# Kernel tuning notes

Hardware: AMD Instinct MI355X
Metric: run time of the kernel (lower is better)

## Reference

```python
import jax, jax.numpy as jnp
import numpy as np

B, D, L, H = 256, 256, 256, 512  # batch, driving series (input_size), (T-1)*features_num, hidden_size


def setup_inputs() -> dict:
    key = jax.random.key(0)
    ks = jax.random.split(key, 6)
    s = 1.0 / np.sqrt(H).astype(np.float32)
    return {
        "input_data": jax.random.normal(ks[0], (B, D, L), jnp.float32),
        # attn_linear: Linear(2H + L -> 1)
        "W_attn": jax.random.normal(ks[1], (2 * H + L, 1), jnp.float32) * 0.02,
        "b_attn": jnp.zeros((1,), jnp.float32),
        # single-layer LSTM params, torch gate order (i, f, g, o)
        "W_ih": jax.random.uniform(ks[2], (4 * H, D), jnp.float32, -s, s),
        "W_hh": jax.random.uniform(ks[3], (4 * H, H), jnp.float32, -s, s),
        "b_ih": jax.random.uniform(ks[4], (4 * H,), jnp.float32, -s, s),
        "b_hh": jnp.zeros((4 * H,), jnp.float32),
    }


def reference(input_data, W_attn, b_attn, W_ih, W_hh, b_ih, b_hh):
    Bn, Dn, Ln = input_data.shape
    Hn = W_hh.shape[1]
    # Split attn weight instead of materializing concat([h, c, x]) each step:
    # score = [h | c | x_hist] @ W_attn + b == h@Wh + c@Wc + x_hist@Wx + b
    Wh = W_attn[:Hn, 0]
    Wc = W_attn[Hn:2 * Hn, 0]
    Wx = W_attn[2 * Hn:, 0]
    # x-history contribution is constant across steps -> hoist out of the scan
    x_proj = jnp.einsum("bdl,l->bd", input_data, Wx) + b_attn[0]  # [B, D]
    bias = b_ih + b_hh
    xs = jnp.moveaxis(input_data, 2, 0)  # [L, B, D] per-step columns x_t

    def step(carry, xt):
        h, c = carry  # [B, H] each
        score = x_proj + (h @ Wh + c @ Wc)[:, None]  # [B, D]
        attn = jax.nn.softmax(score, axis=1)  # softmax over driving series
        w = attn * xt  # attention-weighted input, [B, D]
        gates = w @ W_ih.T + h @ W_hh.T + bias  # [B, 4H]
        i, f, g, o = jnp.split(gates, 4, axis=1)
        c2 = jax.nn.sigmoid(f) * c + jax.nn.sigmoid(i) * jnp.tanh(g)
        h2 = jax.nn.sigmoid(o) * jnp.tanh(c2)
        return (h2, c2), (w, h2)

    h0 = jnp.zeros((Bn, Hn), input_data.dtype)
    c0 = jnp.zeros((Bn, Hn), input_data.dtype)
    _, (ws, hs) = jax.lax.scan(step, (h0, c0), xs)
    # match torch's final permute: [total_x_features, B, *] -> [B, total_x_features, *]
    return jnp.moveaxis(ws, 0, 1), jnp.moveaxis(hs, 0, 1)
```

## Files before the change

### kernel.cpp

```cpp
#include <hip/hip_runtime.h>
#include <hip/hip_fp16.h>

typedef _Float16 half8 __attribute__((ext_vector_type(8)));
typedef float floatx4 __attribute__((ext_vector_type(4)));
typedef int intx4 __attribute__((ext_vector_type(4)));

#define NB 256
#define ND 256
#define NL 256
#define NH 512

__global__ void k_xproj(const float* __restrict__ x, const float* __restrict__ Wattn,
                        float* __restrict__ xproj) {
    __shared__ float wx[NL];
    const int tid = threadIdx.x;
    wx[tid] = Wattn[2 * NH + tid];
    __syncthreads();
    const int wid = tid >> 6, lane = tid & 63;
    const int row = blockIdx.x * 4 + wid;
    const float4 v = ((const float4*)(x + (size_t)row * NL))[lane];
    float s = v.x * wx[lane * 4] + v.y * wx[lane * 4 + 1] +
              v.z * wx[lane * 4 + 2] + v.w * wx[lane * 4 + 3];
    #pragma unroll
    for (int off = 32; off; off >>= 1) s += __shfl_down(s, off);
    if (lane == 0) xproj[row] = s;
}

__global__ void k_softmax(const float* __restrict__ xproj, float* __restrict__ attn) {
    const int b = blockIdx.x, tid = threadIdx.x;
    __shared__ float red[8];
    float v = xproj[b * ND + tid];
    float m = v;
    #pragma unroll
    for (int off = 32; off; off >>= 1) m = fmaxf(m, __shfl_down(m, off));
    const int wid = tid >> 6, lane = tid & 63;
    if (lane == 0) red[wid] = m;
    __syncthreads();
    if (tid == 0) {
        float mm = fmaxf(fmaxf(red[0], red[1]), fmaxf(red[2], red[3]));
        red[4] = mm;
    }
    __syncthreads();
    const float e = expf(v - red[4]);
    float s = e;
    #pragma unroll
    for (int off = 32; off; off >>= 1) s += __shfl_down(s, off);
    if (lane == 0) red[wid] = s;
    __syncthreads();
    if (tid == 0) red[5] = red[0] + red[1] + red[2] + red[3];
    __syncthreads();
    attn[b * ND + tid] = e / red[5];
}

__global__ void k_trans(const float* __restrict__ x, const float* __restrict__ attn,
                        float* __restrict__ ws_out, _Float16* __restrict__ w16) {
    __shared__ float tile[64][65];
    const int bid = blockIdx.x;
    const int b = bid >> 4, ti = (bid >> 2) & 3, tj = bid & 3;
    const int tx = threadIdx.x & 63, ty = threadIdx.x >> 6;
    const int d0 = ti * 64, l0 = tj * 64;
    const float* xb = x + ((size_t)b * ND + d0) * NL + l0;
    #pragma unroll
    for (int r = ty; r < 64; r += 4) tile[r][tx] = xb[(size_t)r * NL + tx];
    __syncthreads();
    const float af = attn[b * ND + d0 + tx];
    #pragma unroll
    for (int r = ty; r < 64; r += 4) {
        const int tt = l0 + r;
        const float val = af * tile[tx][r];
        ws_out[((size_t)b * NL + tt) * ND + d0 + tx] = val;
        w16[((size_t)tt * NB + b) * ND + d0 + tx] = (_Float16)val;
    }
}

__global__ void k_wsplit(const float* __restrict__ Whh, const float* __restrict__ Wih,
                         _Float16* __restrict__ hi, _Float16* __restrict__ lo,
                         _Float16* __restrict__ wih16) {
    const int idx = blockIdx.x * 256 + threadIdx.x;
    const float w = Whh[idx];
    const _Float16 h = (_Float16)w;
    hi[idx] = h;
    lo[idx] = (_Float16)(w - (float)h);
    if (idx < 4 * NH * ND) wih16[idx] = (_Float16)Wih[idx];
}

__launch_bounds__(512, 2)
__global__ void k_recur(const _Float16* __restrict__ whhHi, const _Float16* __restrict__ whhLo,
                        const _Float16* __restrict__ wih16, const _Float16* __restrict__ w16,
                        const float* __restrict__ b_ih, const float* __restrict__ b_hh,
                        unsigned int* __restrict__ h32,
                        float* __restrict__ out_hs)
{
    __shared__ char smem[40960];
    const int tid = threadIdx.x;
    const int wid = tid >> 6, lane = tid & 63;
    const int bid = blockIdx.x;
    const int m = bid & 15, hb = bid >> 4;
    const int b0 = m * 16;
    const int gate = wid >> 1, half = wid & 1;
    const int jb = gate * 512 + hb * 32 + half * 16;

    half8 bhhH[16], bhhL[16], bihF[8];
    const int bcol = jb + (lane & 15);
    const int krow = (lane >> 4) * 8;
    #pragma unroll
    for (int kk = 0; kk < 16; ++kk) {
        bhhH[kk] = *(const half8*)(whhHi + (size_t)bcol * NH + kk * 32 + krow);
        bhhL[kk] = *(const half8*)(whhLo + (size_t)bcol * NH + kk * 32 + krow);
    }
    #pragma unroll
    for (int kk = 0; kk < 8; ++kk)
        bihF[kk] = *(const half8*)(wih16 + (size_t)bcol * ND + kk * 32 + krow);

    const int bl = tid >> 5, hl = tid & 31;
    float bias_[4];
    #pragma unroll
    for (int g = 0; g < 4; ++g) {
        const int j = g * 512 + hb * 32 + hl;
        bias_[g] = b_ih[j] + b_hh[j];
    }
    float c = 0.f;
    float* hsOut = out_hs + (size_t)(b0 + bl) * NL * NH + hb * 32 + hl;
    unsigned int* hWr = h32 + (size_t)(b0 + bl) * NH + hb * 32 + hl;

    const int arow = lane & 15;
    const int aq = (lane >> 4) * 16;
    const int aswz = (arow & 7) << 4;

    const int hrow = tid >> 5;
    const int hcol16 = (tid & 31) * 16;
    const int hbase = (hrow << 10) + (tid & 31) * 32;
    const int hswz = (hrow & 7) << 4;

    {
        const char* wsrc = (const char*)(w16 + (size_t)b0 * ND);
        const intx4 wd = *(const intx4*)(wsrc + tid * 16);
        const int wr = tid >> 5;
        *(intx4*)(smem + 16384 + ((tid * 16) ^ ((wr & 7) << 4))) = wd;
    }
    __syncthreads();

    #pragma unroll 1
    for (int t = 0; t < NL; ++t) {
        const int cur = t & 1, nxt = (t + 1) & 1;

        const int tp = (t + 1 < NL) ? t + 1 : t;
        const intx4 wpref = *(const intx4*)(
            (const char*)(w16 + ((size_t)tp * NB + b0) * ND) + tid * 16);

        floatx4 accC = {0.f, 0.f, 0.f, 0.f};
        #pragma unroll
        for (int kk = 0; kk < 8; ++kk) {
            const int waddr = 16384 + 8192 * cur + ((((arow << 9) + (kk << 6) + aq)) ^ aswz);
            const half8 a = *(const half8*)(smem + waddr);
            accC = __builtin_amdgcn_mfma_f32_16x16x32_f16(a, bihF[kk], accC, 0, 0, 0);
        }

        if (t > 0) {
            const unsigned int* hsrc =
                h32 + (size_t)cur * NB * NH + (size_t)(b0 + hrow) * NH + hcol16;
            intx4 q0, q1, q2, q3;
            const unsigned int et = (unsigned int)t;
            while (true) {
                asm volatile(
                    "global_load_dwordx4 %0, %4, off sc0 sc1\n\t"
                    "global_load_dwordx4 %1, %4, off offset:16 sc0 sc1\n\t"
                    "global_load_dwordx4 %2, %4, off offset:32 sc0 sc1\n\t"
                    "global_load_dwordx4 %3, %4, off offset:48 sc0 sc1\n\t"
                    "s_waitcnt vmcnt(0)"
                    : "=v"(q0), "=v"(q1), "=v"(q2), "=v"(q3)
                    : "v"(hsrc) : "memory");
                bool ok = true;
                #pragma unroll
                for (int i = 0; i < 4; ++i) {
                    ok &= (((unsigned int)q0[i]) >> 16) == et;
                    ok &= (((unsigned int)q1[i]) >> 16) == et;
                    ok &= (((unsigned int)q2[i]) >> 16) == et;
                    ok &= (((unsigned int)q3[i]) >> 16) == et;
                }
                if (ok) break;
            }
            intx4 d0, d1;
            d0[0] = (q0[0] & 0xffff) | (q0[1] << 16);
            d0[1] = (q0[2] & 0xffff) | (q0[3] << 16);
            d0[2] = (q1[0] & 0xffff) | (q1[1] << 16);
            d0[3] = (q1[2] & 0xffff) | (q1[3] << 16);
            d1[0] = (q2[0] & 0xffff) | (q2[1] << 16);
            d1[1] = (q2[2] & 0xffff) | (q2[3] << 16);
            d1[2] = (q3[0] & 0xffff) | (q3[1] << 16);
            d1[3] = (q3[2] & 0xffff) | (q3[3] << 16);
            *(intx4*)(smem + (hbase ^ hswz)) = d0;
            *(intx4*)(smem + ((hbase + 16) ^ hswz)) = d1;
        } else {
            const intx4 z = {0, 0, 0, 0};
            *(intx4*)(smem + (hbase ^ hswz)) = z;
            *(intx4*)(smem + ((hbase + 16) ^ hswz)) = z;
        }
        {
            const int wr = tid >> 5;
            *(intx4*)(smem + 16384 + 8192 * nxt + ((tid * 16) ^ ((wr & 7) << 4))) = wpref;
        }
        __syncthreads();

        floatx4 accA = {0.f, 0.f, 0.f, 0.f};
        floatx4 accB = {0.f, 0.f, 0.f, 0.f};
        #pragma unroll
        for (int kk = 0; kk < 16; ++kk) {
            const int aaddr = ((arow << 10) + (kk << 6) + aq) ^ aswz;
            const half8 a = *(const half8*)(smem + aaddr);
            accA = __builtin_amdgcn_mfma_f32_16x16x32_f16(a, bhhH[kk], accA, 0, 0, 0);
            accB = __builtin_amdgcn_mfma_f32_16x16x32_f16(a, bhhL[kk], accB, 0, 0, 0);
        }
        const floatx4 f = (accA + accB) + accC;

        {
            float* accL = (float*)(smem + 32768);
            const int colw = lane & 15, rowq = (lane >> 4) * 4;
            #pragma unroll
            for (int r = 0; r < 4; ++r)
                accL[wid * 256 + (rowq + r) * 16 + colw] = f[r];
        }
        __syncthreads();

        float h2;
        {
            const float* accL = (const float*)(smem + 32768);
            const int hq = hl >> 4, cidx = hl & 15;
            const int off = bl * 16 + cidx;
            const float pi = accL[(0 + hq) * 256 + off] + bias_[0];
            const float pf = accL[(2 + hq) * 256 + off] + bias_[1];
            const float pg = accL[(4 + hq) * 256 + off] + bias_[2];
            const float po = accL[(6 + hq) * 256 + off] + bias_[3];
            const float si = 1.f / (1.f + __expf(-pi));
            const float sf = 1.f / (1.f + __expf(-pf));
            const float so = 1.f / (1.f + __expf(-po));
            float e2 = __expf(-2.f * fabsf(pg));
            float tg = (1.f - e2) / (1.f + e2);
            tg = (pg < 0.f) ? -tg : tg;
            c = sf * c + si * tg;
            float e2c = __expf(-2.f * fabsf(c));
            float tc = (1.f - e2c) / (1.f + e2c);
            tc = (c < 0.f) ? -tc : tc;
            h2 = so * tc;
            const _Float16 hh = (_Float16)h2;
            const unsigned int hv =
                ((unsigned int)(t + 1) << 16) |
                (unsigned int)__builtin_bit_cast(unsigned short, hh);
            const void* hp = hWr + (size_t)nxt * NB * NH;
            asm volatile("global_store_dword %0, %1, off sc0 sc1"
                         :: "v"(hp), "v"(hv) : "memory");
        }
        hsOut[(size_t)t * NH] = h2;
    }
}

extern "C" void kernel_launch(void* const* d_in, const int* in_sizes, int n_in,
                              void* d_out, int out_size, void* d_ws, size_t ws_size,
                              hipStream_t stream) {
    const float* x     = (const float*)d_in[0];
    const float* Wattn = (const float*)d_in[1];
    const float* Wih   = (const float*)d_in[3];
    const float* Whh   = (const float*)d_in[4];
    const float* bih   = (const float*)d_in[5];
    const float* bhh   = (const float*)d_in[6];

    float* ws_out = (float*)d_out;
    float* hs_out = ws_out + (size_t)NB * NL * ND;

    char* ws = (char*)d_ws;
    float*    attn  = (float*)(ws + 4096);
    float*    xproj = (float*)(ws + 4096 + 262144);
    unsigned int* h32 = (unsigned int*)(ws + 1048576);
    _Float16* whhHi = (_Float16*)(ws + 2097152);
    _Float16* whhLo = (_Float16*)(ws + 2097152 + 2097152);
    _Float16* wih16 = (_Float16*)(ws + 6291456);
    _Float16* w16   = (_Float16*)(ws + 8388608);

    k_xproj  <<<16384, 256, 0, stream>>>(x, Wattn, xproj);
    k_softmax<<<256,   256, 0, stream>>>(xproj, attn);
    k_trans  <<<4096,  256, 0, stream>>>(x, attn, ws_out, w16);
    k_wsplit <<<4096,  256, 0, stream>>>(Whh, Wih, whhHi, whhLo, wih16);
    k_recur  <<<256,   512, 0, stream>>>(whhHi, whhLo, wih16, w16, bih, bhh,
                                         h32, hs_out);
}
```

Measured before the change: 695.8 us.

## Issue h-tag polling loads early, prefetch w two steps ahead, pad gate LDS

The first polling load of the previous step's tagged h values is now issued before the input-projection MFMAs, so its latency overlaps that compute. The spin loop only re-polls on a tag mismatch, and the h read pattern is remapped to two row groups with a new LDS layout. The w prefetch now runs two steps ahead via inline asm, and the gate accumulator staging in LDS is padded to stride 17 to reduce bank conflicts. A memset clears the h/tag buffer so stale tags from earlier runs cannot satisfy the check; it adds a small launch cost and depends on the new layouts and asm scheduling being correct.

```diff
diff --git a/kernel.cpp b/kernel.cpp
--- a/kernel.cpp
+++ b/kernel.cpp
@@ -91,7 +91,7 @@
                         unsigned int* __restrict__ h32,
                         float* __restrict__ out_hs)
 {
-    __shared__ char smem[40960];
+    __shared__ char smem[41472];
     const int tid = threadIdx.x;
     const int wid = tid >> 6, lane = tid & 63;
     const int bid = blockIdx.x;
@@ -101,16 +101,26 @@
     const int jb = gate * 512 + hb * 32 + half * 16;
 
     half8 bhhH[16], bhhL[16], bihF[8];
-    const int bcol = jb + (lane & 15);
-    const int krow = (lane >> 4) * 8;
-    #pragma unroll
-    for (int kk = 0; kk < 16; ++kk) {
-        bhhH[kk] = *(const half8*)(whhHi + (size_t)bcol * NH + kk * 32 + krow);
-        bhhL[kk] = *(const half8*)(whhLo + (size_t)bcol * NH + kk * 32 + krow);
-    }
-    #pragma unroll
-    for (int kk = 0; kk < 8; ++kk)
-        bihF[kk] = *(const half8*)(wih16 + (size_t)bcol * ND + kk * 32 + krow);
+    {
+        const int bcol = jb + (lane & 15);
+        const int krow = (lane >> 4) * 8;
+        const _Float16* ph = whhHi + (size_t)bcol * NH + krow;
+        const _Float16* pl = whhLo + (size_t)bcol * NH + krow;
+        const _Float16* pw = wih16 + (size_t)bcol * ND + krow;
+        #pragma unroll
+        for (int kk = 0; kk < 16; ++kk) {
+            asm volatile("global_load_dwordx4 %0, %1, off"
+                         : "=v"(bhhH[kk]) : "v"(ph + kk * 32));
+            asm volatile("global_load_dwordx4 %0, %1, off"
+                         : "=v"(bhhL[kk]) : "v"(pl + kk * 32));
+        }
+        #pragma unroll
+        for (int kk = 0; kk < 8; ++kk)
+            asm volatile("global_load_dwordx4 %0, %1, off"
+                         : "=v"(bihF[kk]) : "v"(pw + kk * 32));
+        asm volatile("s_waitcnt vmcnt(0)" ::: "memory");
+        __builtin_amdgcn_sched_barrier(0);
+    }
 
     const int bl = tid >> 5, hl = tid & 31;
     float bias_[4];
@@ -127,16 +137,20 @@
     const int aq = (lane >> 4) * 16;
     const int aswz = (arow & 7) << 4;
 
-    const int hrow = tid >> 5;
-    const int hcol16 = (tid & 31) * 16;
-    const int hbase = (hrow << 10) + (tid & 31) * 32;
-    const int hswz = (hrow & 7) << 4;
+    const int r1 = tid >> 6;
+    const int tagoff = (tid & 63) * 8;
+    const int hdst = (tid * 16) ^ (r1 << 4);
+    const int wrow = tid >> 5;
+    const int wdst = (tid * 16) ^ ((wrow & 7) << 4);
 
     {
-        const char* wsrc = (const char*)(w16 + (size_t)b0 * ND);
-        const intx4 wd = *(const intx4*)(wsrc + tid * 16);
-        const int wr = tid >> 5;
-        *(intx4*)(smem + 16384 + ((tid * 16) ^ ((wr & 7) << 4))) = wd;
+        const _Float16* wsrc = w16 + (size_t)(b0 + wrow) * ND + (tid & 31) * 8;
+        *(intx4*)(smem + 16384 + wdst) = *(const intx4*)wsrc;
+    }
+    intx4 wpref;
+    {
+        const _Float16* wsrc = w16 + ((size_t)1 * NB + b0 + wrow) * ND + (tid & 31) * 8;
+        asm volatile("global_load_dwordx4 %0, %1, off" : "=v"(wpref) : "v"(wsrc));
     }
     __syncthreads();
 
@@ -144,33 +158,50 @@
     for (int t = 0; t < NL; ++t) {
         const int cur = t & 1, nxt = (t + 1) & 1;
 
-        const int tp = (t + 1 < NL) ? t + 1 : t;
-        const intx4 wpref = *(const intx4*)(
-            (const char*)(w16 + ((size_t)tp * NB + b0) * ND) + tid * 16);
+        intx4 q0, q1, q2, q3;
+        const unsigned int* p1 =
+            h32 + (size_t)cur * NB * NH + (size_t)(b0 + r1) * NH + tagoff;
+        const unsigned int* p2 = p1 + (size_t)8 * NH;
+        if (t > 0) {
+            asm volatile(
+                "global_load_dwordx4 %0, %4, off sc0 sc1\n\t"
+                "global_load_dwordx4 %1, %4, off offset:16 sc0 sc1\n\t"
+                "global_load_dwordx4 %2, %5, off sc0 sc1\n\t"
+                "global_load_dwordx4 %3, %5, off offset:16 sc0 sc1"
+                : "=v"(q0), "=v"(q1), "=v"(q2), "=v"(q3)
+                : "v"(p1), "v"(p2) : "memory");
+        }
 
         floatx4 accC = {0.f, 0.f, 0.f, 0.f};
         #pragma unroll
         for (int kk = 0; kk < 8; ++kk) {
-            const int waddr = 16384 + 8192 * cur + ((((arow << 9) + (kk << 6) + aq)) ^ aswz);
+            const int waddr = 16384 + 8192 * cur + (((arow << 9) + (kk << 6) + aq) ^ aswz);
             const half8 a = *(const half8*)(smem + waddr);
             accC = __builtin_amdgcn_mfma_f32_16x16x32_f16(a, bihF[kk], accC, 0, 0, 0);
         }
 
         if (t > 0) {
-            const unsigned int* hsrc =
-                h32 + (size_t)cur * NB * NH + (size_t)(b0 + hrow) * NH + hcol16;
-            intx4 q0, q1, q2, q3;
+            asm volatile("s_waitcnt vmcnt(0)" ::: "memory");
+            __builtin_amdgcn_sched_barrier(0);
             const unsigned int et = (unsigned int)t;
-            while (true) {
+            bool ok = true;
+            #pragma unroll
+            for (int i = 0; i < 4; ++i) {
+                ok &= (((unsigned int)q0[i]) >> 16) == et;
+                ok &= (((unsigned int)q1[i]) >> 16) == et;
+                ok &= (((unsigned int)q2[i]) >> 16) == et;
+                ok &= (((unsigned int)q3[i]) >> 16) == et;
+            }
+            while (!ok) {
                 asm volatile(
                     "global_load_dwordx4 %0, %4, off sc0 sc1\n\t"
                     "global_load_dwordx4 %1, %4, off offset:16 sc0 sc1\n\t"
-                    "global_load_dwordx4 %2, %4, off offset:32 sc0 sc1\n\t"
-                    "global_load_dwordx4 %3, %4, off offset:48 sc0 sc1\n\t"
+                    "global_load_dwordx4 %2, %5, off sc0 sc1\n\t"
+                    "global_load_dwordx4 %3, %5, off offset:16 sc0 sc1\n\t"
                     "s_waitcnt vmcnt(0)"
                     : "=v"(q0), "=v"(q1), "=v"(q2), "=v"(q3)
-                    : "v"(hsrc) : "memory");
-                bool ok = true;
+                    : "v"(p1), "v"(p2) : "memory");
+                ok = true;
                 #pragma unroll
                 for (int i = 0; i < 4; ++i) {
                     ok &= (((unsigned int)q0[i]) >> 16) == et;
@@ -178,7 +209,6 @@
                     ok &= (((unsigned int)q2[i]) >> 16) == et;
                     ok &= (((unsigned int)q3[i]) >> 16) == et;
                 }
-                if (ok) break;
             }
             intx4 d0, d1;
             d0[0] = (q0[0] & 0xffff) | (q0[1] << 16);
@@ -189,16 +219,19 @@
             d1[1] = (q2[2] & 0xffff) | (q2[3] << 16);
             d1[2] = (q3[0] & 0xffff) | (q3[1] << 16);
             d1[3] = (q3[2] & 0xffff) | (q3[3] << 16);
-            *(intx4*)(smem + (hbase ^ hswz)) = d0;
-            *(intx4*)(smem + ((hbase + 16) ^ hswz)) = d1;
+            *(intx4*)(smem + hdst) = d0;
+            *(intx4*)(smem + 8192 + hdst) = d1;
         } else {
             const intx4 z = {0, 0, 0, 0};
-            *(intx4*)(smem + (hbase ^ hswz)) = z;
-            *(intx4*)(smem + ((hbase + 16) ^ hswz)) = z;
-        }
+            *(intx4*)(smem + hdst) = z;
+            *(intx4*)(smem + 8192 + hdst) = z;
+        }
+        *(intx4*)(smem + 16384 + 8192 * nxt + wdst) = wpref;
         {
-            const int wr = tid >> 5;
-            *(intx4*)(smem + 16384 + 8192 * nxt + ((tid * 16) ^ ((wr & 7) << 4))) = wpref;
+            const int tp = (t + 2 < NL) ? t + 2 : NL - 1;
+            const _Float16* wsrc =
+                w16 + ((size_t)tp * NB + b0 + wrow) * ND + (tid & 31) * 8;
+            asm volatile("global_load_dwordx4 %0, %1, off" : "=v"(wpref) : "v"(wsrc));
         }
         __syncthreads();
 
@@ -218,7 +251,7 @@
             const int colw = lane & 15, rowq = (lane >> 4) * 4;
             #pragma unroll
             for (int r = 0; r < 4; ++r)
-                accL[wid * 256 + (rowq + r) * 16 + colw] = f[r];
+                accL[wid * 272 + (rowq + r) * 17 + colw] = f[r];
         }
         __syncthreads();
 
@@ -226,11 +259,11 @@
         {
             const float* accL = (const float*)(smem + 32768);
             const int hq = hl >> 4, cidx = hl & 15;
-            const int off = bl * 16 + cidx;
-            const float pi = accL[(0 + hq) * 256 + off] + bias_[0];
-            const float pf = accL[(2 + hq) * 256 + off] + bias_[1];
-            const float pg = accL[(4 + hq) * 256 + off] + bias_[2];
-            const float po = accL[(6 + hq) * 256 + off] + bias_[3];
+            const int off = bl * 17 + cidx;
+            const float pi = accL[(0 + hq) * 272 + off] + bias_[0];
+            const float pf = accL[(2 + hq) * 272 + off] + bias_[1];
+            const float pg = accL[(4 + hq) * 272 + off] + bias_[2];
+            const float po = accL[(6 + hq) * 272 + off] + bias_[3];
             const float si = 1.f / (1.f + __expf(-pi));
             const float sf = 1.f / (1.f + __expf(-pf));
             const float so = 1.f / (1.f + __expf(-po));
@@ -276,6 +309,8 @@
     _Float16* wih16 = (_Float16*)(ws + 6291456);
     _Float16* w16   = (_Float16*)(ws + 8388608);
 
+    hipMemsetAsync(h32, 0, (size_t)2 * NB * NH * 4, stream);
+
     k_xproj  <<<16384, 256, 0, stream>>>(x, Wattn, xproj);
     k_softmax<<<256,   256, 0, stream>>>(xproj, attn);
     k_trans  <<<4096,  256, 0, stream>>>(x, attn, ws_out, w16);
```

Result: slower. 995.5 us (+43.1%).
